# Kernel optimization log

Measured on AMD Instinct MI355X. Metric: run time of the kernel, lower is better.

The kernel has to match this reference:

```python
import jax, jax.numpy as jnp
import numpy as np

S, H, NH, I = 4096, 2048, 16, 5504
HD = H // NH
EPS = 1e-6
ROPE_BASE = 10000.0


def setup_inputs() -> dict:
    key = jax.random.key(0)
    ks = jax.random.split(key, 10)
    sc = lambda fan_in: 1.0 / np.sqrt(fan_in)
    return {
        "x": jax.random.normal(ks[0], (S, H), jnp.float32),
        "wq": jax.random.normal(ks[1], (H, H), jnp.float32) * sc(H),
        "wk": jax.random.normal(ks[2], (H, H), jnp.float32) * sc(H),
        "wv": jax.random.normal(ks[3], (H, H), jnp.float32) * sc(H),
        "wo": jax.random.normal(ks[4], (H, H), jnp.float32) * sc(H),
        "w_gate": jax.random.normal(ks[5], (H, I), jnp.float32) * sc(H),
        "w_up": jax.random.normal(ks[6], (H, I), jnp.float32) * sc(H),
        "w_down": jax.random.normal(ks[7], (I, H), jnp.float32) * sc(I),
        "g1": jnp.ones((H,), jnp.float32),
        "g2": jnp.ones((H,), jnp.float32),
    }


def _rmsnorm(x, g):
    var = jnp.mean(x * x, axis=-1, keepdims=True)
    return x * jax.lax.rsqrt(var + EPS) * g


def _rope(x):
    # x: [S, NH, HD]; classic interleaved-pair rotation applied per position.
    pos = jnp.arange(S, dtype=jnp.float32)
    inv_freq = 1.0 / (ROPE_BASE ** (jnp.arange(0, HD, 2, dtype=jnp.float32) / HD))
    ang = pos[:, None] * inv_freq[None, :]              # [S, HD/2]
    cos = jnp.cos(ang)[:, None, :]                      # [S, 1, HD/2]
    sin = jnp.sin(ang)[:, None, :]
    xe = x[..., 0::2]
    xo = x[..., 1::2]
    out = jnp.stack([xe * cos - xo * sin, xe * sin + xo * cos], axis=-1)
    return out.reshape(x.shape)


def _block(x, wq, wk, wv, wo, w_gate, w_up, w_down, g1, g2):
    # --- attention sublayer ---
    h = _rmsnorm(x, g1)
    q = _rope((h @ wq).reshape(S, NH, HD))
    k = _rope((h @ wk).reshape(S, NH, HD))
    v = (h @ wv).reshape(S, NH, HD)
    scores = jnp.einsum("snd,tnd->nst", q, k) / np.sqrt(HD).astype(np.float32)
    causal = jnp.tril(jnp.ones((S, S), bool))
    scores = jnp.where(causal[None], scores, jnp.finfo(scores.dtype).min)
    probs = jax.nn.softmax(scores, axis=-1)
    attn = jnp.einsum("nst,tnd->snd", probs, v).reshape(S, H)
    x = x + attn @ wo
    # --- MLP sublayer (SwiGLU) ---
    h = _rmsnorm(x, g2)
    mlp = (jax.nn.silu(h @ w_gate) * (h @ w_up)) @ w_down
    return x + mlp


def reference(x, wq, wk, wv, wo, w_gate, w_up, w_down, g1, g2):
    return _block(x, wq, wk, wv, wo, w_gate, w_up, w_down, g1, g2)
```

## Files before the change

### kernel.cpp

```cpp
#include <hip/hip_runtime.h>
#include <stdint.h>

constexpr int SEQ  = 4096;
constexpr int HID  = 2048;
constexpr int NHEAD = 16;
constexpr int HDIM = 128;
constexpr int INTER = 5504;
constexpr int IPAD  = 5632;

using u16 = unsigned short;
typedef __bf16 bf16x8 __attribute__((ext_vector_type(8)));
typedef float  f32x4  __attribute__((ext_vector_type(4)));
typedef u16    u16x4  __attribute__((ext_vector_type(4)));
typedef u16    u16x8  __attribute__((ext_vector_type(8)));

__device__ __forceinline__ u16 f2bf(float f) {
  union { float f; unsigned u; } v; v.f = f;
  return (u16)((v.u + 0x7fffu + ((v.u >> 16) & 1u)) >> 16);
}
__device__ __forceinline__ float bf2f(u16 u) {
  union { unsigned u; float f; } v; v.u = ((unsigned)u) << 16;
  return v.f;
}

__device__ __forceinline__ unsigned cvtpk(float lo, float hi) {
  unsigned r;
  asm("v_cvt_pk_bf16_f32 %0, %1, %2" : "=v"(r) : "v"(lo), "v"(hi));
  return r;
}

__device__ __forceinline__ void gl16(const u16* g, u16* l) {
  u16* gg = const_cast<u16*>(g);
  __builtin_amdgcn_global_load_lds(
      (__attribute__((address_space(1))) u16*)gg,
      (__attribute__((address_space(3))) u16*)l, 16, 0, 0);
}

__device__ __forceinline__ f32x4 mfma16(bf16x8 a, bf16x8 b, f32x4 c) {
  return __builtin_amdgcn_mfma_f32_16x16x32_bf16(a, b, c, 0, 0, 0);
}

__global__ __launch_bounds__(256)
void fill_k(float* __restrict__ o, float v, int n) {
  int i = blockIdx.x * 256 + threadIdx.x;
  if (i < n) o[i] = v;
}

__global__ __launch_bounds__(256)
void rmsnorm_k(const float* __restrict__ x, const float* __restrict__ g,
               u16* __restrict__ o) {
  const int row = blockIdx.x, t = threadIdx.x;
  const float4* xr = (const float4*)(x + (size_t)row * HID);
  float4 a = xr[t * 2], b = xr[t * 2 + 1];
  float ss = a.x*a.x + a.y*a.y + a.z*a.z + a.w*a.w
           + b.x*b.x + b.y*b.y + b.z*b.z + b.w*b.w;
  #pragma unroll
  for (int m = 32; m; m >>= 1) ss += __shfl_xor(ss, m);
  __shared__ float red[4];
  if ((t & 63) == 0) red[t >> 6] = ss;
  __syncthreads();
  const float inv = rsqrtf((red[0]+red[1]+red[2]+red[3]) * (1.0f/HID) + 1e-6f);
  float vals[8] = {a.x,a.y,a.z,a.w,b.x,b.y,b.z,b.w};
  const int base = t * 8;
  u16x8 w;
  #pragma unroll
  for (int i = 0; i < 8; ++i) w[i] = f2bf(vals[i] * inv * g[base + i]);
  *(u16x8*)(o + (size_t)row * HID + base) = w;
}

__global__ __launch_bounds__(256)
void wtrans_k(const float* __restrict__ in, u16* __restrict__ out,
              int ldin, int ldout, int Rin, int Cin) {
  __shared__ float tile[32][33];
  const int cb = blockIdx.x * 32, rb = blockIdx.y * 32;
  const int t = threadIdx.x;
  const int c = t >> 3, r4 = (t & 7) * 4;
  if (rb >= Rin || cb >= Cin) {
    u16x4 z = {0, 0, 0, 0};
    *(u16x4*)(out + (size_t)(cb + c) * ldout + rb + r4) = z;
    return;
  }
  const int r = t >> 3, c4 = (t & 7) * 4;
  float4 v = *(const float4*)(in + (size_t)(rb + r) * ldin + cb + c4);
  tile[r][c4] = v.x; tile[r][c4+1] = v.y; tile[r][c4+2] = v.z; tile[r][c4+3] = v.w;
  __syncthreads();
  u16x4 o;
  #pragma unroll
  for (int i = 0; i < 4; ++i) o[i] = f2bf(tile[r4 + i][c]);
  *(u16x4*)(out + (size_t)(cb + c) * ldout + rb + r4) = o;
}

__global__ __launch_bounds__(256)
void vtrans_k(const u16* __restrict__ v, u16* __restrict__ vt) {
  __shared__ u16 tile[32][36];
  const int s0 = blockIdx.x * 32, d0 = blockIdx.y * 32, n = blockIdx.z;
  const int t = threadIdx.x;
  const int r = t >> 3, c4 = (t & 7) * 4;
  u16x4 in = *(const u16x4*)(v + (size_t)(s0 + r) * HID + n * HDIM + d0 + c4);
  tile[r][c4] = in[0]; tile[r][c4+1] = in[1]; tile[r][c4+2] = in[2]; tile[r][c4+3] = in[3];
  __syncthreads();
  const int d = t >> 3, s4 = (t & 7) * 4;
  u16x4 o;
  #pragma unroll
  for (int i = 0; i < 4; ++i) o[i] = tile[s4 + i][d];
  *(u16x4*)(vt + ((size_t)n * HDIM + d0 + d) * SEQ + s0 + s4) = o;
}

__global__ __launch_bounds__(256)
void rope_k(u16* __restrict__ x) {
  const int idx = blockIdx.x * 256 + threadIdx.x;
  const int i  = idx & 63;
  const int sn = idx >> 6;
  const int s  = sn >> 4;
  const size_t base = (size_t)sn * HDIM + 2 * i;
  const float xe = bf2f(x[base]), xo = bf2f(x[base + 1]);
  const float inv_freq = exp2f(-(float)i * (13.287712379549449f / 64.0f));
  const float ang = (float)s * inv_freq;
  float sv, cv;
  sincosf(ang, &sv, &cv);
  x[base]     = f2bf(xe * cv - xo * sv);
  x[base + 1] = f2bf(xe * sv + xo * cv);
}

template<int EPI>
__global__ __launch_bounds__(256)
void gemm128(const u16* __restrict__ A, const u16* __restrict__ B,
             void* C, const void* extra, int M, int N, int K, int gx) {
  __shared__ __align__(16) u16 As[128 * 64];
  __shared__ __align__(16) u16 Bs[128 * 64];
  const int nwg = gridDim.x;
  const int bid = blockIdx.x;
  const int wgid = (bid & 7) * (nwg >> 3) + (bid >> 3);
  const int bx = wgid % gx, by = wgid / gx;
  const int m0 = by * 128, n0 = bx * 128;
  const int tid = threadIdx.x;
  const int w = tid >> 6, lane = tid & 63;
  const int l15 = lane & 15, g = lane >> 4;
  const int wr = w >> 1, wc = w & 1;
  const int NT = K >> 6;

  f32x4 acc[4][4] = {};

  const int srow = tid >> 3;
  const int sgr  = ((tid & 7) ^ (srow & 7)) * 8;
  const u16* gA = A + (size_t)(m0 + srow) * K + sgr;
  const u16* gB = B + (size_t)(n0 + srow) * K + sgr;
  const size_t i32K = (size_t)32 * K;
  const int sl = w * 512;

  const int axor = l15 & 7;
  const int arow0 = (wr * 64 + l15) * 64;
  const int brow0 = (wc * 64 + l15) * 64;

  for (int T = 0; T < NT; ++T) {
    const size_t k0 = (size_t)T * 64;
    gl16(gA + k0,            As + 0 * 2048 + sl);
    gl16(gA + k0 +     i32K, As + 1 * 2048 + sl);
    gl16(gA + k0 + 2 * i32K, As + 2 * 2048 + sl);
    gl16(gA + k0 + 3 * i32K, As + 3 * 2048 + sl);
    gl16(gB + k0,            Bs + 0 * 2048 + sl);
    gl16(gB + k0 +     i32K, Bs + 1 * 2048 + sl);
    gl16(gB + k0 + 2 * i32K, Bs + 2 * 2048 + sl);
    gl16(gB + k0 + 3 * i32K, Bs + 3 * 2048 + sl);
    asm volatile("s_waitcnt vmcnt(0)" ::: "memory");
    __syncthreads();
    #pragma unroll
    for (int ks = 0; ks < 2; ++ks) {
      const int aoff = ((ks * 4 + g) ^ axor) * 8;
      bf16x8 af[4], bfr[4];
      #pragma unroll
      for (int i = 0; i < 4; ++i)
        af[i] = *(const bf16x8*)&As[arow0 + i * 16 * 64 + aoff];
      #pragma unroll
      for (int j = 0; j < 4; ++j)
        bfr[j] = *(const bf16x8*)&Bs[brow0 + j * 16 * 64 + aoff];
      #pragma unroll
      for (int i = 0; i < 4; ++i)
        #pragma unroll
        for (int j = 0; j < 4; ++j)
          acc[i][j] = mfma16(af[i], bfr[j], acc[i][j]);
    }
    asm volatile("s_waitcnt lgkmcnt(0)" ::: "memory");
    __syncthreads();
  }

  #pragma unroll
  for (int i = 0; i < 4; ++i) {
    #pragma unroll
    for (int r = 0; r < 4; ++r) {
      const int row = m0 + wr * 64 + i * 16 + g * 4 + r;
      #pragma unroll
      for (int j = 0; j < 4; ++j) {
        const int col = n0 + wc * 64 + j * 16 + l15;
        const float v = acc[i][j][r];
        if constexpr (EPI == 0) {
          ((u16*)C)[(size_t)(col >> 11) * ((size_t)SEQ * HID)
                    + (size_t)row * HID + (col & 2047)] = f2bf(v);
        } else if constexpr (EPI == 1) {
          const size_t idx = (size_t)row * N + col;
          ((float*)C)[idx] = v + ((const float*)extra)[idx];
        } else if constexpr (EPI == 2) {
          const size_t idx = (size_t)row * N + col;
          const float upv = bf2f(((const u16*)extra)[idx]);
          ((u16*)C)[idx] = f2bf(v / (1.0f + __expf(-v)) * upv);
        } else {
          ((u16*)C)[(size_t)row * N + col] = f2bf(v);
        }
      }
    }
  }
}

__global__ __launch_bounds__(256)
void attn_k(const u16* __restrict__ q, const u16* __restrict__ k,
            const u16* __restrict__ vt, u16* __restrict__ o) {
  __shared__ __align__(16) u16 Ks[64 * 128];
  __shared__ __align__(16) u16 Vs[128 * 64];
  __shared__ __align__(16) u16 Ps[4 * 16 * 64];
  const int b = blockIdx.x;
  const int n    = ((b & 7) << 1) | ((b >> 3) & 1);
  const int qIdx = 63 - (b >> 4);
  const int q0   = qIdx * 64;
  const int tid = threadIdx.x;
  const int wave = tid >> 6, lane = tid & 63;
  const int l15 = lane & 15, g = lane >> 4;

  bf16x8 aq[4];
  {
    const u16* qp = q + (size_t)(q0 + wave*16 + l15) * HID + n * HDIM + g * 8;
    #pragma unroll
    for (int d = 0; d < 4; ++d) aq[d] = *(const bf16x8*)(qp + d * 32);
  }
  float mrow[4];
  #pragma unroll
  for (int r = 0; r < 4; ++r) mrow[r] = -__builtin_inff();
  f32x4 oacc[8] = {};
  f32x4 lacc = {0.0f, 0.0f, 0.0f, 0.0f};
  const bf16x8 vone = {(__bf16)1.0f, (__bf16)1.0f, (__bf16)1.0f, (__bf16)1.0f,
                       (__bf16)1.0f, (__bf16)1.0f, (__bf16)1.0f, (__bf16)1.0f};

  const int kRow = tid >> 4;
  const int kCs  = (tid & 15) ^ (kRow & 7);
  const u16* kg = k + (size_t)kRow * HID + n * HDIM + kCs * 8;
  const int vRow = tid >> 3;
  const int vCs  = (tid & 7) ^ (vRow & 7);
  const u16* vg = vt + ((size_t)n * HDIM + vRow) * SEQ + vCs * 8;

  u16* PW = Ps + wave * 1024;
  const int rsw = (l15 & 7) << 3;
  const float C = 0.12751744f;

  const int nt = qIdx + 1;
  for (int it = 0; it < nt; ++it) {
    const int t0 = it * 64;
    #pragma unroll
    for (int s = 0; s < 4; ++s)
      gl16(kg + (size_t)(t0 + s*16) * HID, Ks + s*2048 + wave*512);
    #pragma unroll
    for (int s = 0; s < 4; ++s)
      gl16(vg + (size_t)(s*32) * SEQ + t0, Vs + s*2048 + wave*512);
    asm volatile("s_waitcnt vmcnt(0)" ::: "memory");
    __syncthreads();

    f32x4 sc[4] = {};
    #pragma unroll
    for (int tb = 0; tb < 4; ++tb) {
      #pragma unroll
      for (int dd = 0; dd < 4; ++dd) {
        bf16x8 bk = *(const bf16x8*)(Ks + (tb*16 + l15)*128 + ((dd*32 + g*8) ^ rsw));
        sc[tb] = mfma16(aq[dd], bk, sc[tb]);
      }
    }

    const bool diag = (it == qIdx);
    #pragma unroll
    for (int r = 0; r < 4; ++r) {
      float v0 = sc[0][r], v1 = sc[1][r], v2 = sc[2][r], v3 = sc[3][r];
      if (diag) {
        const int srow = q0 + wave*16 + g*4 + r;
        const int tt = t0 + l15;
        if (tt      > srow) v0 = -__builtin_inff();
        if (tt + 16 > srow) v1 = -__builtin_inff();
        if (tt + 32 > srow) v2 = -__builtin_inff();
        if (tt + 48 > srow) v3 = -__builtin_inff();
      }
      float mx = fmaxf(fmaxf(v0, v1), fmaxf(v2, v3));
      mx = fmaxf(mx, __shfl_xor(mx, 1));
      mx = fmaxf(mx, __shfl_xor(mx, 2));
      mx = fmaxf(mx, __shfl_xor(mx, 4));
      mx = fmaxf(mx, __shfl_xor(mx, 8));
      if (mx > mrow[r] + 60.0f) {
        const float f = exp2f((mrow[r] - mx) * C);
        mrow[r] = mx;
        lacc[r] *= f;
        #pragma unroll
        for (int db = 0; db < 8; ++db) oacc[db][r] *= f;
      }
      const float m = mrow[r];
      const float p0 = exp2f((v0 - m) * C);
      const float p1 = exp2f((v1 - m) * C);
      const float p2 = exp2f((v2 - m) * C);
      const float p3 = exp2f((v3 - m) * C);
      const unsigned pk01 = cvtpk(p0, p1);
      const unsigned pk23 = cvtpk(p2, p3);
      const int prow = g*4 + r;
      const int psw = (prow & 7) << 3;
      PW[prow*64 + ( l15        ^ psw)] = (u16)pk01;
      PW[prow*64 + ((16 + l15)  ^ psw)] = (u16)(pk01 >> 16);
      PW[prow*64 + ((32 + l15)  ^ psw)] = (u16)pk23;
      PW[prow*64 + ((48 + l15)  ^ psw)] = (u16)(pk23 >> 16);
    }

    bf16x8 ap0 = *(const bf16x8*)(PW + l15*64 + ((g*8)      ^ rsw));
    bf16x8 ap1 = *(const bf16x8*)(PW + l15*64 + ((32 + g*8) ^ rsw));
    lacc = mfma16(ap0, vone, lacc);
    lacc = mfma16(ap1, vone, lacc);
    #pragma unroll
    for (int db = 0; db < 8; ++db) {
      bf16x8 bv0 = *(const bf16x8*)(Vs + (db*16 + l15)*64 + ((g*8)      ^ rsw));
      bf16x8 bv1 = *(const bf16x8*)(Vs + (db*16 + l15)*64 + ((32 + g*8) ^ rsw));
      oacc[db] = mfma16(ap0, bv0, oacc[db]);
      oacc[db] = mfma16(ap1, bv1, oacc[db]);
    }
    asm volatile("s_waitcnt lgkmcnt(0)" ::: "memory");
    __syncthreads();
  }

  #pragma unroll
  for (int db = 0; db < 8; ++db) {
    #pragma unroll
    for (int r = 0; r < 4; ++r) {
      const int srow = q0 + wave*16 + g*4 + r;
      o[(size_t)srow * HID + n * HDIM + db*16 + l15] = f2bf(oacc[db][r] / lacc[r]);
    }
  }
}

extern "C" void kernel_launch(void* const* d_in, const int* in_sizes, int n_in,
                              void* d_out, int out_size, void* d_ws, size_t ws_size,
                              hipStream_t stream) {
  (void)in_sizes; (void)n_in; (void)out_size;
  const float* x  = (const float*)d_in[0];
  const float* wq = (const float*)d_in[1];
  const float* wk = (const float*)d_in[2];
  const float* wv = (const float*)d_in[3];
  const float* wo = (const float*)d_in[4];
  const float* wg = (const float*)d_in[5];
  const float* wu = (const float*)d_in[6];
  const float* wd = (const float*)d_in[7];
  const float* g1 = (const float*)d_in[8];
  const float* g2 = (const float*)d_in[9];
  float* out = (float*)d_out;

  constexpr size_t HB  = (size_t)SEQ * HID * 2;
  constexpr size_t WT  = (size_t)HID * HID * 2;
  constexpr size_t WUP = (size_t)IPAD * HID * 2;
  constexpr size_t UPH = (size_t)SEQ * IPAD * 2;
  constexpr size_t NEED1 = 4 * HB + 3 * WT;
  constexpr size_t NEED2 = HB + WUP + UPH;
  constexpr size_t NEED = NEED1 > NEED2 ? NEED1 : NEED2;

  if (ws_size < NEED) {
    const int n = SEQ * HID;
    fill_k<<<dim3((n + 255) / 256), 256, 0, stream>>>(out, (float)(ws_size >> 20), n);
    return;
  }

  char* base = (char*)d_ws;
  u16* h1     = (u16*)(base);
  u16* wqkvT  = (u16*)(base + HB);
  u16* qb     = (u16*)(base + HB + 3 * WT);
  u16* kb     = (u16*)(base + 2 * HB + 3 * WT);
  u16* vb     = (u16*)(base + 3 * HB + 3 * WT);
  u16* vtb    = h1;
  u16* ob     = vb;
  u16* woT    = wqkvT;
  u16* h2    = (u16*)(base);
  u16* slotA = (u16*)(base + HB);
  u16* uph   = (u16*)(base + HB + WUP);

  wtrans_k<<<dim3(64, 64), 256, 0, stream>>>(wq, wqkvT,            HID, HID, HID, HID);
  wtrans_k<<<dim3(64, 64), 256, 0, stream>>>(wk, wqkvT + HID*HID,  HID, HID, HID, HID);
  wtrans_k<<<dim3(64, 64), 256, 0, stream>>>(wv, wqkvT + 2*HID*HID,HID, HID, HID, HID);

  rmsnorm_k<<<dim3(SEQ), 256, 0, stream>>>(x, g1, h1);

  gemm128<0><<<dim3(1536), 256, 0, stream>>>(h1, wqkvT, qb, nullptr, SEQ, 3*HID, HID, 48);

  rope_k<<<dim3(SEQ * NHEAD * 64 / 256), 256, 0, stream>>>(qb);
  rope_k<<<dim3(SEQ * NHEAD * 64 / 256), 256, 0, stream>>>(kb);

  vtrans_k<<<dim3(SEQ/32, HDIM/32, NHEAD), 256, 0, stream>>>(vb, vtb);

  wtrans_k<<<dim3(64, 64), 256, 0, stream>>>(wo, woT, HID, HID, HID, HID);

  attn_k<<<dim3(SEQ/64 * NHEAD), 256, 0, stream>>>(qb, kb, vtb, ob);

  gemm128<1><<<dim3(512), 256, 0, stream>>>(ob, woT, out, x, SEQ, HID, HID, 16);

  rmsnorm_k<<<dim3(SEQ), 256, 0, stream>>>(out, g2, h2);

  wtrans_k<<<dim3(IPAD/32, 64), 256, 0, stream>>>(wu, slotA, INTER, HID, HID, INTER);
  gemm128<3><<<dim3(1408), 256, 0, stream>>>(h2, slotA, uph, nullptr, SEQ, IPAD, HID, 44);

  wtrans_k<<<dim3(IPAD/32, 64), 256, 0, stream>>>(wg, slotA, INTER, HID, HID, INTER);
  gemm128<2><<<dim3(1408), 256, 0, stream>>>(h2, slotA, uph, uph, SEQ, IPAD, HID, 44);

  wtrans_k<<<dim3(64, IPAD/32), 256, 0, stream>>>(wd, slotA, HID, IPAD, INTER, HID);
  gemm128<1><<<dim3(512), 256, 0, stream>>>(uph, slotA, out, out, SEQ, HID, IPAD, 16);
}
```

Before: 858.0 us.

## Double-buffer K/V tiles and widen attention blocks to 128 query rows

The attention kernel now uses 8 waves covering 128 query rows per block, so each K/V tile loaded into shared memory is reused by twice as many queries. K/V loads are double-buffered: the next tile is prefetched while the current one is consumed, overlapping global loads with MFMA work. The causal mask now applies per wave based on row range. It doubles LDS usage and grid shrinks to 512 blocks, which may reduce occupancy and load balance.

```diff
diff --git a/kernel.cpp b/kernel.cpp
--- a/kernel.cpp
+++ b/kernel.cpp
@@ -211,23 +211,24 @@
   }
 }
 
-__global__ __launch_bounds__(256)
+__global__ __launch_bounds__(512, 4)
 void attn_k(const u16* __restrict__ q, const u16* __restrict__ k,
             const u16* __restrict__ vt, u16* __restrict__ o) {
-  __shared__ __align__(16) u16 Ks[64 * 128];
-  __shared__ __align__(16) u16 Vs[128 * 64];
-  __shared__ __align__(16) u16 Ps[4 * 16 * 64];
+  __shared__ __align__(16) u16 Ks[2][64 * 128];
+  __shared__ __align__(16) u16 Vs[2][128 * 64];
+  __shared__ __align__(16) u16 Ps[8 * 16 * 64];
   const int b = blockIdx.x;
-  const int n    = ((b & 7) << 1) | ((b >> 3) & 1);
-  const int qIdx = 63 - (b >> 4);
-  const int q0   = qIdx * 64;
+  const int n  = ((b & 7) << 1) | ((b >> 3) & 1);
+  const int qI = 31 - (b >> 4);
+  const int q0 = qI * 128;
   const int tid = threadIdx.x;
   const int wave = tid >> 6, lane = tid & 63;
   const int l15 = lane & 15, g = lane >> 4;
+  const int qw = q0 + wave * 16;
 
   bf16x8 aq[4];
   {
-    const u16* qp = q + (size_t)(q0 + wave*16 + l15) * HID + n * HDIM + g * 8;
+    const u16* qp = q + (size_t)(qw + l15) * HID + n * HDIM + g * 8;
     #pragma unroll
     for (int d = 0; d < 4; ++d) aq[d] = *(const bf16x8*)(qp + d * 32);
   }
@@ -246,38 +247,46 @@
   const int vCs  = (tid & 7) ^ (vRow & 7);
   const u16* vg = vt + ((size_t)n * HDIM + vRow) * SEQ + vCs * 8;
 
+#define STAGE(buf, t0_) do { \
+    gl16(kg + (size_t)(t0_) * HID,        &Ks[buf][wave * 512]); \
+    gl16(kg + (size_t)((t0_) + 32) * HID, &Ks[buf][4096 + wave * 512]); \
+    gl16(vg + (t0_),                      &Vs[buf][wave * 512]); \
+    gl16(vg + (size_t)64 * SEQ + (t0_),   &Vs[buf][4096 + wave * 512]); \
+  } while (0)
+
   u16* PW = Ps + wave * 1024;
   const int rsw = (l15 & 7) << 3;
   const float C = 0.12751744f;
 
-  const int nt = qIdx + 1;
+  const int nt = 2 * qI + 2;
+
+  STAGE(0, 0);
+  asm volatile("s_waitcnt vmcnt(0)" ::: "memory");
+  __syncthreads();
+
   for (int it = 0; it < nt; ++it) {
+    const int cur = it & 1;
     const int t0 = it * 64;
-    #pragma unroll
-    for (int s = 0; s < 4; ++s)
-      gl16(kg + (size_t)(t0 + s*16) * HID, Ks + s*2048 + wave*512);
-    #pragma unroll
-    for (int s = 0; s < 4; ++s)
-      gl16(vg + (size_t)(s*32) * SEQ + t0, Vs + s*2048 + wave*512);
-    asm volatile("s_waitcnt vmcnt(0)" ::: "memory");
-    __syncthreads();
+    if (it + 1 < nt) STAGE(cur ^ 1, t0 + 64);
+    const u16* KS = Ks[cur];
+    const u16* VS = Vs[cur];
 
     f32x4 sc[4] = {};
     #pragma unroll
     for (int tb = 0; tb < 4; ++tb) {
       #pragma unroll
       for (int dd = 0; dd < 4; ++dd) {
-        bf16x8 bk = *(const bf16x8*)(Ks + (tb*16 + l15)*128 + ((dd*32 + g*8) ^ rsw));
+        bf16x8 bk = *(const bf16x8*)(KS + (tb*16 + l15)*128 + ((dd*32 + g*8) ^ rsw));
         sc[tb] = mfma16(aq[dd], bk, sc[tb]);
       }
     }
 
-    const bool diag = (it == qIdx);
+    const bool needmask = (t0 + 63 > qw);
     #pragma unroll
     for (int r = 0; r < 4; ++r) {
       float v0 = sc[0][r], v1 = sc[1][r], v2 = sc[2][r], v3 = sc[3][r];
-      if (diag) {
-        const int srow = q0 + wave*16 + g*4 + r;
+      if (needmask) {
+        const int srow = qw + g*4 + r;
         const int tt = t0 + l15;
         if (tt      > srow) v0 = -__builtin_inff();
         if (tt + 16 > srow) v1 = -__builtin_inff();
@@ -317,20 +326,22 @@
     lacc = mfma16(ap1, vone, lacc);
     #pragma unroll
     for (int db = 0; db < 8; ++db) {
-      bf16x8 bv0 = *(const bf16x8*)(Vs + (db*16 + l15)*64 + ((g*8)      ^ rsw));
-      bf16x8 bv1 = *(const bf16x8*)(Vs + (db*16 + l15)*64 + ((32 + g*8) ^ rsw));
+      bf16x8 bv0 = *(const bf16x8*)(VS + (db*16 + l15)*64 + ((g*8)      ^ rsw));
+      bf16x8 bv1 = *(const bf16x8*)(VS + (db*16 + l15)*64 + ((32 + g*8) ^ rsw));
       oacc[db] = mfma16(ap0, bv0, oacc[db]);
       oacc[db] = mfma16(ap1, bv1, oacc[db]);
     }
+    asm volatile("s_waitcnt vmcnt(0)" ::: "memory");
     asm volatile("s_waitcnt lgkmcnt(0)" ::: "memory");
     __syncthreads();
   }
+#undef STAGE
 
   #pragma unroll
   for (int db = 0; db < 8; ++db) {
     #pragma unroll
     for (int r = 0; r < 4; ++r) {
-      const int srow = q0 + wave*16 + g*4 + r;
+      const int srow = qw + g*4 + r;
       o[(size_t)srow * HID + n * HDIM + db*16 + l15] = f2bf(oacc[db][r] / lacc[r]);
     }
   }
@@ -394,7 +405,7 @@
 
   wtrans_k<<<dim3(64, 64), 256, 0, stream>>>(wo, woT, HID, HID, HID, HID);
 
-  attn_k<<<dim3(SEQ/64 * NHEAD), 256, 0, stream>>>(qb, kb, vtb, ob);
+  attn_k<<<dim3(512), 512, 0, stream>>>(qb, kb, vtb, ob);
 
   gemm128<1><<<dim3(512), 256, 0, stream>>>(ob, woT, out, x, SEQ, HID, HID, 16);
 
```

New measurement: 876.8 us. 2.2% more time.
